# Optimization experiments

Hardware: AMD Instinct MI355X
Metric: run time of the kernel (lower is better)

## Reference

```python
import jax, jax.numpy as jnp
import numpy as np

N = 4096
IN_DIM = 256
OUT_DIM = 256
NUM_HEADS = 4
HEAD_DIM = OUT_DIM // NUM_HEADS


def setup_inputs() -> dict:
    key = jax.random.key(0)
    ks = jax.random.split(key, 10)
    x = jax.random.normal(ks[0], (N, IN_DIM), dtype=jnp.float32)
    adj = jax.random.randint(ks[1], (N, N), 0, 2, dtype=jnp.int32)
    adj = jnp.maximum(adj, jnp.eye(N, dtype=jnp.int32))  # self-loops -> no empty rows
    s_in = 1.0 / np.sqrt(IN_DIM)
    s_out = 1.0 / np.sqrt(OUT_DIM)
    Wq = jax.random.uniform(ks[2], (IN_DIM, OUT_DIM), jnp.float32, -s_in, s_in)
    bq = jnp.zeros((OUT_DIM,), jnp.float32)
    Wk = jax.random.uniform(ks[3], (IN_DIM, OUT_DIM), jnp.float32, -s_in, s_in)
    bk = jnp.zeros((OUT_DIM,), jnp.float32)
    Wv = jax.random.uniform(ks[4], (IN_DIM, OUT_DIM), jnp.float32, -s_in, s_in)
    bv = jnp.zeros((OUT_DIM,), jnp.float32)
    Wo = jax.random.uniform(ks[5], (OUT_DIM, OUT_DIM), jnp.float32, -s_out, s_out)
    bo = jnp.zeros((OUT_DIM,), jnp.float32)
    gamma = jnp.ones((OUT_DIM,), jnp.float32)
    beta = jnp.zeros((OUT_DIM,), jnp.float32)
    return {"x": x, "adj": adj, "Wq": Wq, "bq": bq, "Wk": Wk, "bk": bk,
            "Wv": Wv, "bv": bv, "Wo": Wo, "bo": bo, "gamma": gamma, "beta": beta}


def layer_norm(h, gamma, beta, eps=1e-5):
    mu = jnp.mean(h, axis=-1, keepdims=True)
    var = jnp.mean(jnp.square(h - mu), axis=-1, keepdims=True)
    return (h - mu) * jax.lax.rsqrt(var + eps) * gamma + beta


def reference(x, adj, Wq, bq, Wk, bk, Wv, bv, Wo, bo, gamma, beta):
    n = x.shape[0]
    q_proj = x @ Wq + bq                       # (N, out_dim), reused for residual
    Q = q_proj.reshape(n, NUM_HEADS, HEAD_DIM)
    K = (x @ Wk + bk).reshape(n, NUM_HEADS, HEAD_DIM)
    V = (x @ Wv + bv).reshape(n, NUM_HEADS, HEAD_DIM)
    scores = jnp.einsum('nhd,mhd->nmh', Q, K) / np.sqrt(HEAD_DIM)
    scores = jnp.where(adj[:, :, None] == 0, -jnp.inf, scores)
    attn = jax.nn.softmax(scores, axis=1)      # softmax over neighbor axis m
    out = jnp.einsum('nmh,mhd->nhd', attn, V).reshape(n, OUT_DIM)
    out = out @ Wo + bo
    return layer_norm(out + q_proj, gamma, beta)
```

## Files before the change

kernel.cpp:

```cpp
#include <hip/hip_runtime.h>
#include <math.h>

#define NN 4096
#define DIM 256
#define NHEADS 4
#define HDIM 64

typedef short bf16x8 __attribute__((ext_vector_type(8)));
typedef float f32x4  __attribute__((ext_vector_type(4)));

__device__ __forceinline__ unsigned short f2bf(float f) {
    unsigned int u = __float_as_uint(f);
    u += 0x7fffu + ((u >> 16) & 1u);
    return (unsigned short)(u >> 16);
}
__device__ __forceinline__ float bf2f(unsigned short h) {
    return __uint_as_float(((unsigned int)h) << 16);
}
__device__ __forceinline__ void async16(const void* g, void* l) {
    __builtin_amdgcn_global_load_lds(
        (const __attribute__((address_space(1))) unsigned int*)g,
        (__attribute__((address_space(3))) unsigned int*)l, 16, 0, 0);
}

__global__ __launch_bounds__(256)
void prep_kernel(const float* __restrict__ W0, const float* __restrict__ W1,
                 const float* __restrict__ W2, const float* __restrict__ W3,
                 unsigned short* __restrict__ T0, unsigned short* __restrict__ T1,
                 unsigned short* __restrict__ T2, unsigned short* __restrict__ T3)
{
    __shared__ unsigned short Ts[64][65];
    const int b = blockIdx.x, t = threadIdx.x;
    const int mat = b >> 4, tile = b & 15;
    const int r0 = (tile >> 2) * 64, c0 = (tile & 3) * 64;
    const float* W = (mat == 0) ? W0 : (mat == 1) ? W1 : (mat == 2) ? W2 : W3;
    unsigned short* T = (mat == 0) ? T0 : (mat == 1) ? T1 : (mat == 2) ? T2 : T3;
    {
        int r = t >> 2, c4 = (t & 3) * 16;
        #pragma unroll
        for (int j = 0; j < 4; ++j) {
            float4 v = *reinterpret_cast<const float4*>(W + (size_t)(r0 + r) * DIM + c0 + c4 + j * 4);
            Ts[c4 + j * 4 + 0][r] = f2bf(v.x);
            Ts[c4 + j * 4 + 1][r] = f2bf(v.y);
            Ts[c4 + j * 4 + 2][r] = f2bf(v.z);
            Ts[c4 + j * 4 + 3][r] = f2bf(v.w);
        }
    }
    __syncthreads();
    {
        int d = t >> 2, k4 = (t & 3) * 16;
        #pragma unroll
        for (int j = 0; j < 4; ++j) {
            ushort4 u;
            u.x = Ts[d][k4 + j * 4 + 0];
            u.y = Ts[d][k4 + j * 4 + 1];
            u.z = Ts[d][k4 + j * 4 + 2];
            u.w = Ts[d][k4 + j * 4 + 3];
            *reinterpret_cast<ushort4*>(T + (size_t)(c0 + d) * DIM + r0 + k4 + j * 4) = u;
        }
    }
}

__global__ __launch_bounds__(256)
void qkv_mask(const float* __restrict__ x,
              const unsigned short* __restrict__ WqT, const unsigned short* __restrict__ WkT,
              const unsigned short* __restrict__ WvT,
              const float* __restrict__ bq, const float* __restrict__ bk, const float* __restrict__ bv,
              unsigned short* __restrict__ Qo, unsigned short* __restrict__ Ko,
              unsigned short* __restrict__ VTo,
              const int* __restrict__ adj, unsigned long long* __restrict__ maskT)
{
    const int b = blockIdx.x, t = threadIdx.x, w = t >> 6, l = t & 63;

    if (b >= 384) {
        const int ww = (b - 384) * 4 + w;
        for (int idx = ww; idx < 65536; idx += 8192) {
            const int row = idx >> 4, st = idx & 15;
            const int4 a = *reinterpret_cast<const int4*>(adj + (size_t)row * NN + st * 256 + l * 4);
            unsigned long long b0 = __ballot(a.x != 0);
            unsigned long long b1 = __ballot(a.y != 0);
            unsigned long long b2 = __ballot(a.z != 0);
            unsigned long long b3 = __ballot(a.w != 0);
            if (l < 4) {
                unsigned long long bb = (l == 0) ? b0 : (l == 1) ? b1 : (l == 2) ? b2 : b3;
                maskT[(size_t)row * 64 + st * 4 + l] = bb;
            }
        }
        return;
    }

    const int l15 = l & 15, lg = l >> 4;
    const int which = b >> 7, xb = b & 127;
    const int row0 = xb * 32 + (w >> 1) * 16;
    const int col0 = (w & 1) * 128;
    const unsigned short* WT; const float* bias;
    if (which == 0)      { WT = WqT; bias = bq; }
    else if (which == 1) { WT = WkT; bias = bk; }
    else                 { WT = WvT; bias = bv; }

    f32x4 acc[8] = {};
    for (int k0 = 0; k0 < DIM; k0 += 32) {
        const float* xp = x + (size_t)(row0 + l15) * DIM + k0 + lg * 8;
        float4 x0 = *reinterpret_cast<const float4*>(xp);
        float4 x1 = *reinterpret_cast<const float4*>(xp + 4);
        union { unsigned u[4]; bf16x8 v; } xa;
        asm("v_cvt_pk_bf16_f32 %0, %1, %2" : "=v"(xa.u[0]) : "v"(x0.x), "v"(x0.y));
        asm("v_cvt_pk_bf16_f32 %0, %1, %2" : "=v"(xa.u[1]) : "v"(x0.z), "v"(x0.w));
        asm("v_cvt_pk_bf16_f32 %0, %1, %2" : "=v"(xa.u[2]) : "v"(x1.x), "v"(x1.y));
        asm("v_cvt_pk_bf16_f32 %0, %1, %2" : "=v"(xa.u[3]) : "v"(x1.z), "v"(x1.w));
        #pragma unroll
        for (int nt = 0; nt < 8; ++nt) {
            bf16x8 wb = *(const bf16x8*)(WT + (size_t)(col0 + nt * 16 + l15) * DIM + k0 + lg * 8);
            acc[nt] = __builtin_amdgcn_mfma_f32_16x16x32_bf16(xa.v, wb, acc[nt], 0, 0, 0);
        }
    }
    #pragma unroll
    for (int nt = 0; nt < 8; ++nt) {
        int col = col0 + nt * 16 + l15;
        float bb = bias[col];
        #pragma unroll
        for (int r = 0; r < 4; ++r) {
            int row = row0 + lg * 4 + r;
            float ov = acc[nt][r] + bb;
            if (which == 1) ov *= 0.18033688f;
            unsigned short val = f2bf(ov);
            if (which == 2) {
                int rb = row & 63;
                int vnt = rb >> 4, vlg = (rb >> 2) & 3, vr = rb & 3;
                int pos = ((vnt & 1) << 5) | (vlg << 3) | ((vnt >> 1) << 2) | vr;
                VTo[(size_t)col * NN + ((row & ~63) | pos)] = val;
            } else if (which == 0) Qo[(size_t)row * DIM + col] = val;
            else                   Ko[(size_t)row * DIM + col] = val;
        }
    }
}

template<int NTILES>
__global__ __launch_bounds__(256)
void attn_mfma(const unsigned short* __restrict__ Qb, const unsigned short* __restrict__ Kb,
               const unsigned short* __restrict__ VT, const unsigned long long* __restrict__ maskT,
               unsigned short* __restrict__ Opart, float* __restrict__ lpart)
{
    constexpr int NSTR = NTILES / 4;
    __shared__ unsigned short Kt[3][64][64];
    __shared__ unsigned short Vt[3][64][64];

    const int t = threadIdx.x, w = t >> 6, l = t & 63, l15 = l & 15, lg = l >> 4;
    const int n0 = blockIdx.x * 64, h = blockIdx.y, sp = blockIdx.z;
    const int kv_base = sp * NTILES * 64;
    const int qrow = n0 + w * 16;

    const unsigned short* qp = Qb + (size_t)(qrow + l15) * DIM + h * HDIM + lg * 8;
    const bf16x8 qa0 = *(const bf16x8*)(qp);
    const bf16x8 qa1 = *(const bf16x8*)(qp + 32);

    const unsigned long long* mbase = maskT + (size_t)(qrow + l15) * 64 + (kv_base >> 6);

    const int srow  = w * 16 + (l >> 3);
    const int sunit = (l & 7) ^ (srow & 7);
    const unsigned short* kS = Kb + (size_t)(kv_base + srow) * DIM + h * HDIM + sunit * 8;
    const unsigned short* vS = VT + (size_t)(h * HDIM + srow) * NN + kv_base + sunit * 8;

    const int xr  = l15 & 7;
    const int ko0 = (lg ^ xr) << 4;
    const int ko1 = ((4 + lg) ^ xr) << 4;

    f32x4 oa[4] = {};
    float lsum = 0.f;

    #pragma unroll
    for (int pt = 0; pt < 2; ++pt) {
        unsigned short* kd = &Kt[pt][w * 16][0];
        unsigned short* vd = &Vt[pt][w * 16][0];
        const unsigned short* ks = kS + (size_t)pt * 64 * DIM;
        const unsigned short* vs = vS + pt * 64;
        async16(ks, kd); async16(ks + 8 * DIM, kd + 8 * 64);
        async16(vs, vd); async16(vs + 8 * NN,  vd + 8 * 64);
    }

    #pragma unroll
    for (int st = 0; st < NSTR; ++st) {
        const ulonglong4 m4 = *reinterpret_cast<const ulonglong4*>(mbase + st * 4);
        const unsigned lo[4] = {(unsigned)m4.x, (unsigned)m4.y, (unsigned)m4.z, (unsigned)m4.w};
        const unsigned hi[4] = {(unsigned)(m4.x >> 32), (unsigned)(m4.y >> 32),
                                (unsigned)(m4.z >> 32), (unsigned)(m4.w >> 32)};

        #pragma unroll
        for (int m = 0; m < 4; ++m) {
            const int tl = st * 4 + m;
            if (tl < NTILES - 1) asm volatile("s_waitcnt vmcnt(4)" ::: "memory");
            else                 asm volatile("s_waitcnt vmcnt(0)" ::: "memory");
            __builtin_amdgcn_s_barrier();
            __builtin_amdgcn_sched_barrier(0);

            if (tl + 2 < NTILES) {
                const int bb = (tl + 2) % 3;
                unsigned short* kd = &Kt[bb][w * 16][0];
                unsigned short* vd = &Vt[bb][w * 16][0];
                const unsigned short* ks = kS + (size_t)(tl + 2) * 64 * DIM;
                const unsigned short* vs = vS + (tl + 2) * 64;
                async16(ks, kd); async16(ks + 8 * DIM, kd + 8 * 64);
                async16(vs, vd); async16(vs + 8 * NN,  vd + 8 * 64);
            }

            const int cb = tl % 3;
            const char* kbase = (const char*)&Kt[cb][0][0] + l15 * 128;
            const char* vbase = (const char*)&Vt[cb][0][0] + l15 * 128;

            f32x4 sa[4] = {};
            __builtin_amdgcn_s_setprio(1);
            #pragma unroll
            for (int nt = 0; nt < 4; ++nt) {
                bf16x8 kb0 = *(const bf16x8*)(kbase + nt * 2048 + ko0);
                bf16x8 kb1 = *(const bf16x8*)(kbase + nt * 2048 + ko1);
                sa[nt] = __builtin_amdgcn_mfma_f32_16x16x32_bf16(kb0, qa0, sa[nt], 0, 0, 0);
                sa[nt] = __builtin_amdgcn_mfma_f32_16x16x32_bf16(kb1, qa1, sa[nt], 0, 0, 0);
            }
            __builtin_amdgcn_s_setprio(0);

            const int bsh = ((m & 1) << 4) + lg;
            const unsigned s0 = ((m & 2) ? hi[0] : lo[0]) >> bsh;
            const unsigned s1 = ((m & 2) ? hi[1] : lo[1]) >> bsh;
            const unsigned s2 = ((m & 2) ? hi[2] : lo[2]) >> bsh;
            const unsigned s3 = ((m & 2) ? hi[3] : lo[3]) >> bsh;
            float p[4][4];
            #pragma unroll
            for (int nt = 0; nt < 4; ++nt) {
                p[nt][0] = exp2f(((s0 >> (nt * 4)) & 1u) ? sa[nt][0] : -INFINITY);
                p[nt][1] = exp2f(((s1 >> (nt * 4)) & 1u) ? sa[nt][1] : -INFINITY);
                p[nt][2] = exp2f(((s2 >> (nt * 4)) & 1u) ? sa[nt][2] : -INFINITY);
                p[nt][3] = exp2f(((s3 >> (nt * 4)) & 1u) ? sa[nt][3] : -INFINITY);
            }
            lsum += (((p[0][0] + p[0][1]) + (p[0][2] + p[0][3])) +
                     ((p[1][0] + p[1][1]) + (p[1][2] + p[1][3]))) +
                    (((p[2][0] + p[2][1]) + (p[2][2] + p[2][3])) +
                     ((p[3][0] + p[3][1]) + (p[3][2] + p[3][3])));
            union { unsigned u[4]; bf16x8 v; } a0, a1;
            asm("v_cvt_pk_bf16_f32 %0, %1, %2" : "=v"(a0.u[0]) : "v"(p[0][0]), "v"(p[0][1]));
            asm("v_cvt_pk_bf16_f32 %0, %1, %2" : "=v"(a0.u[1]) : "v"(p[0][2]), "v"(p[0][3]));
            asm("v_cvt_pk_bf16_f32 %0, %1, %2" : "=v"(a0.u[2]) : "v"(p[2][0]), "v"(p[2][1]));
            asm("v_cvt_pk_bf16_f32 %0, %1, %2" : "=v"(a0.u[3]) : "v"(p[2][2]), "v"(p[2][3]));
            asm("v_cvt_pk_bf16_f32 %0, %1, %2" : "=v"(a1.u[0]) : "v"(p[1][0]), "v"(p[1][1]));
            asm("v_cvt_pk_bf16_f32 %0, %1, %2" : "=v"(a1.u[1]) : "v"(p[1][2]), "v"(p[1][3]));
            asm("v_cvt_pk_bf16_f32 %0, %1, %2" : "=v"(a1.u[2]) : "v"(p[3][0]), "v"(p[3][1]));
            asm("v_cvt_pk_bf16_f32 %0, %1, %2" : "=v"(a1.u[3]) : "v"(p[3][2]), "v"(p[3][3]));
            const bf16x8 pa0 = a0.v;
            const bf16x8 pa1 = a1.v;

            __builtin_amdgcn_s_setprio(1);
            #pragma unroll
            for (int nt = 0; nt < 4; ++nt) {
                bf16x8 vb0 = *(const bf16x8*)(vbase + nt * 2048 + ko0);
                bf16x8 vb1 = *(const bf16x8*)(vbase + nt * 2048 + ko1);
                oa[nt] = __builtin_amdgcn_mfma_f32_16x16x32_bf16(pa0, vb0, oa[nt], 0, 0, 0);
                oa[nt] = __builtin_amdgcn_mfma_f32_16x16x32_bf16(pa1, vb1, oa[nt], 0, 0, 0);
            }
            __builtin_amdgcn_s_setprio(0);
        }
    }

    {
        float v = lsum;
        v += __shfl_xor(v, 16);
        v += __shfl_xor(v, 32);
        if (lg == 0)
            lpart[((size_t)sp * NN + qrow + l15) * NHEADS + h] = v;
    }
    #pragma unroll
    for (int r = 0; r < 4; ++r) {
        const int qr = qrow + lg * 4 + r;
        #pragma unroll
        for (int nt = 0; nt < 4; ++nt)
            Opart[((size_t)sp * NN + qr) * DIM + h * HDIM + nt * 16 + l15] = f2bf(oa[nt][r]);
    }
}

__global__ __launch_bounds__(256)
void combine_kernel(const unsigned short* __restrict__ Opart, const float* __restrict__ lpart,
                    unsigned short* __restrict__ AOb, int S)
{
    const int tid = blockIdx.x * blockDim.x + threadIdx.x;
    const int q  = tid >> 6;
    const int d  = (tid & 63) * 4;
    const int h  = d >> 6;
    float o0 = 0.f, o1 = 0.f, o2 = 0.f, o3 = 0.f, lsum = 0.f;
    for (int s = 0; s < S; ++s) {
        ushort4 u = *reinterpret_cast<const ushort4*>(Opart + ((size_t)s * NN + q) * DIM + d);
        o0 += bf2f(u.x); o1 += bf2f(u.y); o2 += bf2f(u.z); o3 += bf2f(u.w);
        lsum += lpart[((size_t)s * NN + q) * NHEADS + h];
    }
    float inv = 1.f / lsum;
    ushort4 o;
    o.x = f2bf(o0 * inv); o.y = f2bf(o1 * inv); o.z = f2bf(o2 * inv); o.w = f2bf(o3 * inv);
    *reinterpret_cast<ushort4*>(AOb + (size_t)q * DIM + d) = o;
}

__global__ __launch_bounds__(256)
void out_ln(const unsigned short* __restrict__ Ab, const unsigned short* __restrict__ WoT,
            const float* __restrict__ bo, const unsigned short* __restrict__ Rb,
            const float* __restrict__ gamma, const float* __restrict__ beta,
            float* __restrict__ out)
{
    __shared__ float redsum[4][16];
    __shared__ float redsq[4][16];
    const int t = threadIdx.x, w = t >> 6, l = t & 63, l15 = l & 15, lg = l >> 4;
    const int row0 = blockIdx.x * 16;
    const int col0 = w * 64;

    f32x4 acc[4] = {};
    for (int k0 = 0; k0 < DIM; k0 += 32) {
        bf16x8 xa = *(const bf16x8*)(Ab + (size_t)(row0 + l15) * DIM + k0 + lg * 8);
        #pragma unroll
        for (int nt = 0; nt < 4; ++nt) {
            bf16x8 wb = *(const bf16x8*)(WoT + (size_t)(col0 + nt * 16 + l15) * DIM + k0 + lg * 8);
            acc[nt] = __builtin_amdgcn_mfma_f32_16x16x32_bf16(xa, wb, acc[nt], 0, 0, 0);
        }
    }

    float psum[4] = {0, 0, 0, 0}, psq[4] = {0, 0, 0, 0};
    #pragma unroll
    for (int nt = 0; nt < 4; ++nt) {
        int col = col0 + nt * 16 + l15;
        float bb = bo[col];
        #pragma unroll
        for (int r = 0; r < 4; ++r) {
            int row = row0 + lg * 4 + r;
            float xv = acc[nt][r] + bb + bf2f(Rb[(size_t)row * DIM + col]);
            acc[nt][r] = xv;
            psum[r] += xv; psq[r] += xv * xv;
        }
    }
    #pragma unroll
    for (int r = 0; r < 4; ++r) {
        float s = psum[r], q = psq[r];
        s += __shfl_xor(s, 1); q += __shfl_xor(q, 1);
        s += __shfl_xor(s, 2); q += __shfl_xor(q, 2);
        s += __shfl_xor(s, 4); q += __shfl_xor(q, 4);
        s += __shfl_xor(s, 8); q += __shfl_xor(q, 8);
        psum[r] = s; psq[r] = q;
    }
    if (l15 == 0) {
        #pragma unroll
        for (int r = 0; r < 4; ++r) {
            redsum[w][lg * 4 + r] = psum[r];
            redsq[w][lg * 4 + r]  = psq[r];
        }
    }
    __syncthreads();

    float msave[4], rsave[4];
    #pragma unroll
    for (int r = 0; r < 4; ++r) {
        int row = lg * 4 + r;
        float s = redsum[0][row] + redsum[1][row] + redsum[2][row] + redsum[3][row];
        float q = redsq[0][row] + redsq[1][row] + redsq[2][row] + redsq[3][row];
        float mean = s * (1.f / 256.f);
        float var  = q * (1.f / 256.f) - mean * mean;
        msave[r] = mean;
        rsave[r] = rsqrtf(var + 1e-5f);
    }
    #pragma unroll
    for (int nt = 0; nt < 4; ++nt) {
        int col = col0 + nt * 16 + l15;
        float g = gamma[col], bt = beta[col];
        #pragma unroll
        for (int r = 0; r < 4; ++r) {
            int row = row0 + lg * 4 + r;
            out[(size_t)row * DIM + col] = (acc[nt][r] - msave[r]) * rsave[r] * g + bt;
        }
    }
}

extern "C" void kernel_launch(void* const* d_in, const int* in_sizes, int n_in,
                              void* d_out, int out_size, void* d_ws, size_t ws_size,
                              hipStream_t stream) {
    const float* x     = (const float*)d_in[0];
    const int*   adj   = (const int*)  d_in[1];
    const float* Wq    = (const float*)d_in[2];
    const float* bq    = (const float*)d_in[3];
    const float* Wk    = (const float*)d_in[4];
    const float* bk    = (const float*)d_in[5];
    const float* Wv    = (const float*)d_in[6];
    const float* bv    = (const float*)d_in[7];
    const float* Wo    = (const float*)d_in[8];
    const float* bo    = (const float*)d_in[9];
    const float* gamma = (const float*)d_in[10];
    const float* beta  = (const float*)d_in[11];
    float* out = (float*)d_out;

    char* ws = (char*)d_ws;
    const size_t MB = 1u << 20;
    unsigned short*     Qb    = (unsigned short*)(ws + 0 * MB);
    unsigned short*     Kb    = (unsigned short*)(ws + 2 * MB);
    unsigned short*     VT    = (unsigned short*)(ws + 4 * MB);
    unsigned long long* maskT = (unsigned long long*)(ws + 6 * MB);
    unsigned short*     WqT   = (unsigned short*)(ws + 8 * MB);
    unsigned short*     WkT   = (unsigned short*)(ws + 8 * MB + 128 * 1024);
    unsigned short*     WvT   = (unsigned short*)(ws + 8 * MB + 256 * 1024);
    unsigned short*     WoT   = (unsigned short*)(ws + 8 * MB + 384 * 1024);
    unsigned short*     AOb   = (unsigned short*)(ws + 8 * MB + 512 * 1024);
    float*              lpart = (float*)(ws + 10 * MB + 512 * 1024);
    unsigned short*     Opart = (unsigned short*)(ws + 11 * MB);

    const int S = (ws_size >= 27 * MB) ? 8 : 4;

    prep_kernel<<<64, 256, 0, stream>>>(Wq, Wk, Wv, Wo, WqT, WkT, WvT, WoT);

    qkv_mask<<<384 + 2048, 256, 0, stream>>>(
        x, WqT, WkT, WvT, bq, bk, bv, Qb, Kb, VT, adj, maskT);

    if (S == 8)
        attn_mfma<8><<<dim3(NN / 64, NHEADS, 8), 256, 0, stream>>>(
            Qb, Kb, VT, maskT, Opart, lpart);
    else
        attn_mfma<16><<<dim3(NN / 64, NHEADS, 4), 256, 0, stream>>>(
            Qb, Kb, VT, maskT, Opart, lpart);

    combine_kernel<<<NN * DIM / 4 / 256, 256, 0, stream>>>(Opart, lpart, AOb, S);

    out_ln<<<NN / 16, 256, 0, stream>>>(AOb, WoT, bo, Qb, gamma, beta, out);
}
```

Before: 88.27 us.

## Rework attention split, buffering, mask layout and row-sum via MFMA

The mask builder now has each lane read strided ints, so every ballot covers a contiguous 64-column run and the bit layout changes to match. The attention kernel goes from triple to double buffering with a full vmcnt(0) wait, and sets launch bounds for 8 blocks per CU. Its grid is flattened to 1D with a swizzle so that consecutive blocks cover different heads and splits of the same query block, and the split count is fixed at 4. The softmax row sum is now computed by an extra MFMA against a ones vector instead of scalar adds and shuffles. The aim is lower LDS use, higher occupancy, better cache locality and fewer VALU ops, at the cost of less load-ahead depth and a fixed split.

Result: faster. 85.30 us (-3.4%).

```diff
diff --git a/kernel.cpp b/kernel.cpp
--- a/kernel.cpp
+++ b/kernel.cpp
@@ -76,11 +76,15 @@
         const int ww = (b - 384) * 4 + w;
         for (int idx = ww; idx < 65536; idx += 8192) {
             const int row = idx >> 4, st = idx & 15;
-            const int4 a = *reinterpret_cast<const int4*>(adj + (size_t)row * NN + st * 256 + l * 4);
-            unsigned long long b0 = __ballot(a.x != 0);
-            unsigned long long b1 = __ballot(a.y != 0);
-            unsigned long long b2 = __ballot(a.z != 0);
-            unsigned long long b3 = __ballot(a.w != 0);
+            const int* ap = adj + (size_t)row * NN + st * 256 + l;
+            const int a0 = ap[0];
+            const int a1 = ap[64];
+            const int a2 = ap[128];
+            const int a3 = ap[192];
+            unsigned long long b0 = __ballot(a0 != 0);
+            unsigned long long b1 = __ballot(a1 != 0);
+            unsigned long long b2 = __ballot(a2 != 0);
+            unsigned long long b3 = __ballot(a3 != 0);
             if (l < 4) {
                 unsigned long long bb = (l == 0) ? b0 : (l == 1) ? b1 : (l == 2) ? b2 : b3;
                 maskT[(size_t)row * 64 + st * 4 + l] = bb;
@@ -136,17 +140,22 @@
 }
 
 template<int NTILES>
-__global__ __launch_bounds__(256)
+__global__ __launch_bounds__(256, 8)
 void attn_mfma(const unsigned short* __restrict__ Qb, const unsigned short* __restrict__ Kb,
                const unsigned short* __restrict__ VT, const unsigned long long* __restrict__ maskT,
                unsigned short* __restrict__ Opart, float* __restrict__ lpart)
 {
     constexpr int NSTR = NTILES / 4;
-    __shared__ unsigned short Kt[3][64][64];
-    __shared__ unsigned short Vt[3][64][64];
+    __shared__ unsigned short Kt[2][64][64];
+    __shared__ unsigned short Vt[2][64][64];
 
     const int t = threadIdx.x, w = t >> 6, l = t & 63, l15 = l & 15, lg = l >> 4;
-    const int n0 = blockIdx.x * 64, h = blockIdx.y, sp = blockIdx.z;
+    const int bid = blockIdx.x;
+    const int slice = (bid & 7) + 8 * (bid >> 9);
+    const int qb    = (bid >> 3) & 63;
+    const int h  = slice & 3;
+    const int sp = slice >> 2;
+    const int n0 = qb * 64;
     const int kv_base = sp * NTILES * 64;
     const int qrow = n0 + w * 16;
 
@@ -165,45 +174,41 @@
     const int ko0 = (lg ^ xr) << 4;
     const int ko1 = ((4 + lg) ^ xr) << 4;
 
+    const short onev = (l15 == 0) ? (short)0x3F80 : (short)0;
+    const bf16x8 onesb = {onev, onev, onev, onev, onev, onev, onev, onev};
+
     f32x4 oa[4] = {};
-    float lsum = 0.f;
-
-    #pragma unroll
-    for (int pt = 0; pt < 2; ++pt) {
-        unsigned short* kd = &Kt[pt][w * 16][0];
-        unsigned short* vd = &Vt[pt][w * 16][0];
-        const unsigned short* ks = kS + (size_t)pt * 64 * DIM;
-        const unsigned short* vs = vS + pt * 64;
-        async16(ks, kd); async16(ks + 8 * DIM, kd + 8 * 64);
-        async16(vs, vd); async16(vs + 8 * NN,  vd + 8 * 64);
-    }
-
-    #pragma unroll
+    f32x4 os = {};
+
+    {
+        unsigned short* kd = &Kt[0][w * 16][0];
+        unsigned short* vd = &Vt[0][w * 16][0];
+        async16(kS, kd); async16(kS + 8 * DIM, kd + 8 * 64);
+        async16(vS, vd); async16(vS + 8 * NN,  vd + 8 * 64);
+    }
+
+    #pragma unroll 1
     for (int st = 0; st < NSTR; ++st) {
         const ulonglong4 m4 = *reinterpret_cast<const ulonglong4*>(mbase + st * 4);
-        const unsigned lo[4] = {(unsigned)m4.x, (unsigned)m4.y, (unsigned)m4.z, (unsigned)m4.w};
-        const unsigned hi[4] = {(unsigned)(m4.x >> 32), (unsigned)(m4.y >> 32),
-                                (unsigned)(m4.z >> 32), (unsigned)(m4.w >> 32)};
 
         #pragma unroll
         for (int m = 0; m < 4; ++m) {
             const int tl = st * 4 + m;
-            if (tl < NTILES - 1) asm volatile("s_waitcnt vmcnt(4)" ::: "memory");
-            else                 asm volatile("s_waitcnt vmcnt(0)" ::: "memory");
+            asm volatile("s_waitcnt vmcnt(0)" ::: "memory");
             __builtin_amdgcn_s_barrier();
             __builtin_amdgcn_sched_barrier(0);
 
-            if (tl + 2 < NTILES) {
-                const int bb = (tl + 2) % 3;
+            if (tl + 1 < NTILES) {
+                const int bb = (tl + 1) & 1;
                 unsigned short* kd = &Kt[bb][w * 16][0];
                 unsigned short* vd = &Vt[bb][w * 16][0];
-                const unsigned short* ks = kS + (size_t)(tl + 2) * 64 * DIM;
-                const unsigned short* vs = vS + (tl + 2) * 64;
+                const unsigned short* ks = kS + (size_t)(tl + 1) * 64 * DIM;
+                const unsigned short* vs = vS + (tl + 1) * 64;
                 async16(ks, kd); async16(ks + 8 * DIM, kd + 8 * 64);
                 async16(vs, vd); async16(vs + 8 * NN,  vd + 8 * 64);
             }
 
-            const int cb = tl % 3;
+            const int cb = tl & 1;
             const char* kbase = (const char*)&Kt[cb][0][0] + l15 * 128;
             const char* vbase = (const char*)&Vt[cb][0][0] + l15 * 128;
 
@@ -218,23 +223,21 @@
             }
             __builtin_amdgcn_s_setprio(0);
 
-            const int bsh = ((m & 1) << 4) + lg;
-            const unsigned s0 = ((m & 2) ? hi[0] : lo[0]) >> bsh;
-            const unsigned s1 = ((m & 2) ? hi[1] : lo[1]) >> bsh;
-            const unsigned s2 = ((m & 2) ? hi[2] : lo[2]) >> bsh;
-            const unsigned s3 = ((m & 2) ? hi[3] : lo[3]) >> bsh;
+            const unsigned long long w64 =
+                (m == 0) ? m4.x : (m == 1) ? m4.y : (m == 2) ? m4.z : m4.w;
+            const unsigned long long sh = w64 >> (lg * 4);
+            const unsigned shlo = (unsigned)sh, shhi = (unsigned)(sh >> 32);
             float p[4][4];
             #pragma unroll
             for (int nt = 0; nt < 4; ++nt) {
-                p[nt][0] = exp2f(((s0 >> (nt * 4)) & 1u) ? sa[nt][0] : -INFINITY);
-                p[nt][1] = exp2f(((s1 >> (nt * 4)) & 1u) ? sa[nt][1] : -INFINITY);
-                p[nt][2] = exp2f(((s2 >> (nt * 4)) & 1u) ? sa[nt][2] : -INFINITY);
-                p[nt][3] = exp2f(((s3 >> (nt * 4)) & 1u) ? sa[nt][3] : -INFINITY);
+                #pragma unroll
+                for (int r = 0; r < 4; ++r) {
+                    const int bitpos = nt * 16 + r;
+                    const unsigned word = (bitpos < 32) ? shlo : shhi;
+                    const unsigned bit = (word >> (bitpos & 31)) & 1u;
+                    p[nt][r] = exp2f(bit ? sa[nt][r] : -INFINITY);
+                }
             }
-            lsum += (((p[0][0] + p[0][1]) + (p[0][2] + p[0][3])) +
-                     ((p[1][0] + p[1][1]) + (p[1][2] + p[1][3]))) +
-                    (((p[2][0] + p[2][1]) + (p[2][2] + p[2][3])) +
-                     ((p[3][0] + p[3][1]) + (p[3][2] + p[3][3])));
             union { unsigned u[4]; bf16x8 v; } a0, a1;
             asm("v_cvt_pk_bf16_f32 %0, %1, %2" : "=v"(a0.u[0]) : "v"(p[0][0]), "v"(p[0][1]));
             asm("v_cvt_pk_bf16_f32 %0, %1, %2" : "=v"(a0.u[1]) : "v"(p[0][2]), "v"(p[0][3]));
@@ -255,23 +258,20 @@
                 oa[nt] = __builtin_amdgcn_mfma_f32_16x16x32_bf16(pa0, vb0, oa[nt], 0, 0, 0);
                 oa[nt] = __builtin_amdgcn_mfma_f32_16x16x32_bf16(pa1, vb1, oa[nt], 0, 0, 0);
             }
+            os = __builtin_amdgcn_mfma_f32_16x16x32_bf16(pa0, onesb, os, 0, 0, 0);
+            os = __builtin_amdgcn_mfma_f32_16x16x32_bf16(pa1, onesb, os, 0, 0, 0);
             __builtin_amdgcn_s_setprio(0);
         }
     }
 
-    {
-        float v = lsum;
-        v += __shfl_xor(v, 16);
-        v += __shfl_xor(v, 32);
-        if (lg == 0)
-            lpart[((size_t)sp * NN + qrow + l15) * NHEADS + h] = v;
-    }
     #pragma unroll
     for (int r = 0; r < 4; ++r) {
         const int qr = qrow + lg * 4 + r;
         #pragma unroll
         for (int nt = 0; nt < 4; ++nt)
             Opart[((size_t)sp * NN + qr) * DIM + h * HDIM + nt * 16 + l15] = f2bf(oa[nt][r]);
+        if (l15 == 0)
+            lpart[((size_t)sp * NN + qr) * NHEADS + h] = os[r];
     }
 }
 
@@ -402,19 +402,14 @@
     float*              lpart = (float*)(ws + 10 * MB + 512 * 1024);
     unsigned short*     Opart = (unsigned short*)(ws + 11 * MB);
 
-    const int S = (ws_size >= 27 * MB) ? 8 : 4;
+    const int S = 4;
 
     prep_kernel<<<64, 256, 0, stream>>>(Wq, Wk, Wv, Wo, WqT, WkT, WvT, WoT);
 
     qkv_mask<<<384 + 2048, 256, 0, stream>>>(
         x, WqT, WkT, WvT, bq, bk, bv, Qb, Kb, VT, adj, maskT);
 
-    if (S == 8)
-        attn_mfma<8><<<dim3(NN / 64, NHEADS, 8), 256, 0, stream>>>(
-            Qb, Kb, VT, maskT, Opart, lpart);
-    else
-        attn_mfma<16><<<dim3(NN / 64, NHEADS, 4), 256, 0, stream>>>(
-            Qb, Kb, VT, maskT, Opart, lpart);
+    attn_mfma<16><<<1024, 256, 0, stream>>>(Qb, Kb, VT, maskT, Opart, lpart);
 
     combine_kernel<<<NN * DIM / 4 / 256, 256, 0, stream>>>(Opart, lpart, AOb, S);
 
```
